# Performance work log

Hardware: AMD Instinct MI355X
Metric: run time of the kernel (lower is better)

## Reference

```python
import jax, jax.numpy as jnp
import numpy as np

V_IPC, N_ROLES, D = 50000, 16, 256
B, L = 2048, 64
F_BIB, H1, H2, D_OUT = 512, 1024, 1024, 512
N_EXP, N_CLS = 8, 10
LN_EPS = 1e-5


def setup_inputs() -> dict:
    key = jax.random.key(0)
    ks = jax.random.split(key, 24)
    s = 0.05
    ipc_emb = jax.random.normal(ks[0], (V_IPC, D), jnp.float32) * s
    ipc_emb = ipc_emb.at[0].set(0.0)  # padding_idx=0
    role_emb = jax.random.normal(ks[1], (N_ROLES, D), jnp.float32) * s
    role_emb = role_emb.at[0].set(0.0)
    inp = {
        "ipc_indices": jax.random.randint(ks[2], (B, L), 0, V_IPC),
        "role_indices": jax.random.randint(ks[3], (B, L), 0, N_ROLES),
        "bibliometric_features": jax.random.normal(ks[4], (B, F_BIB), jnp.float32),
        "ipc_padding_mask": jax.random.randint(ks[5], (B, L), 0, 2).astype(jnp.int32),
        "top_k": 2,
        "ipc_emb": ipc_emb,
        "role_emb": role_emb,
        "Wq": jax.random.normal(ks[6], (D, D), jnp.float32) * s,
        "bq": jnp.zeros((D,), jnp.float32),
        "Wk": jax.random.normal(ks[7], (D, D), jnp.float32) * s,
        "bk": jnp.zeros((D,), jnp.float32),
        "Wv": jax.random.normal(ks[8], (D, D), jnp.float32) * s,
        "bv": jnp.zeros((D,), jnp.float32),
        "global_context": jax.random.normal(ks[9], (D,), jnp.float32) * s,
        "ln_g": jnp.ones((D,), jnp.float32),
        "ln_b": jnp.zeros((D,), jnp.float32),
        "gate_W": jax.random.normal(ks[10], (D, N_EXP), jnp.float32) * s,
        "gate_b": jnp.zeros((N_EXP,), jnp.float32),
        "expert_biases": jnp.zeros((N_EXP,), jnp.float32),
        "W1": jax.random.normal(ks[11], (N_EXP, F_BIB, H1), jnp.float32) * s,
        "b1": jnp.zeros((N_EXP, H1), jnp.float32),
        "W2": jax.random.normal(ks[12], (N_EXP, H1, H2), jnp.float32) * s,
        "b2": jnp.zeros((N_EXP, H2), jnp.float32),
        "W3": jax.random.normal(ks[13], (N_EXP, H2, D_OUT), jnp.float32) * s,
        "b3": jnp.zeros((N_EXP, D_OUT), jnp.float32),
        "head_W": jax.random.normal(ks[14], (D_OUT, N_CLS), jnp.float32) * s,
        "head_b": jnp.zeros((N_CLS,), jnp.float32),
    }
    return inp


def reference(ipc_indices, role_indices, bibliometric_features, ipc_padding_mask, top_k,
              ipc_emb, role_emb, Wq, bq, Wk, bk, Wv, bv, global_context, ln_g, ln_b,
              gate_W, gate_b, expert_biases, W1, b1, W2, b2, W3, b3, head_W, head_b):
    # embeddings + role combine  -> [B, L, D]
    x = ipc_emb[ipc_indices] + role_emb[role_indices]
    # attention pooling with a global learned query (same query for every batch row)
    keys = x @ Wk + bk                                  # [B, L, D]
    values = x @ Wv + bv                                # [B, L, D]
    q = global_context @ Wq + bq                        # [D]
    scores = jnp.einsum('d,bld->bl', q, keys)           # [B, L]
    scores = jnp.where(ipc_padding_mask == 0, -1e9, scores)
    attn = jax.nn.softmax(scores, axis=-1)              # [B, L]
    pooled = jnp.einsum('bl,bld->bd', attn, values)     # [B, D]
    mu = pooled.mean(-1, keepdims=True)
    var = ((pooled - mu) ** 2).mean(-1, keepdims=True)
    router_in = (pooled - mu) / jnp.sqrt(var + LN_EPS) * ln_g + ln_b
    # router: select with biased scores, gate with unbiased scores
    affinity = router_in @ gate_W + gate_b              # [B, E]
    sel_scores = affinity + expert_biases
    _, idx = jax.lax.top_k(sel_scores, top_k)           # [B, K]
    gw = jax.nn.softmax(jnp.take_along_axis(affinity, idx, axis=-1), axis=-1)  # [B, K]
    # dense all-expert MLP (reference form of masked per-expert loop)
    h = jax.nn.relu(jnp.einsum('bi,eih->ebh', bibliometric_features, W1) + b1[:, None, :])
    h = jax.nn.relu(jnp.einsum('ebh,ehj->ebj', h, W2) + b2[:, None, :])
    eo = jnp.einsum('ebj,ejo->ebo', h, W3) + b3[:, None, :]  # [E, B, O]
    # gather each token's top-k expert outputs and combine
    bidx = jnp.arange(idx.shape[0])[:, None]            # [B, 1]
    sel_out = eo[idx, bidx]                             # [B, K, O]
    moe_out = jnp.einsum('bk,bko->bo', gw, sel_out)     # [B, O]
    logits = moe_out @ head_W + head_b                  # [B, n_classes]
    return logits, idx
```

## Files before the change

kernel.cpp:

```cpp
#include <hip/hip_runtime.h>
#include <hip/hip_bf16.h>
#include <math.h>


#define LN_EPS 1e-5f

typedef __bf16 bf16_t;
typedef __bf16 bf16x8 __attribute__((ext_vector_type(8)));
typedef float f32x4 __attribute__((ext_vector_type(4)));

__global__ __launch_bounds__(256)
void prep_kq(const float* __restrict__ Wq, const float* __restrict__ bq,
             const float* __restrict__ Wk, const float* __restrict__ bk,
             const float* __restrict__ gc, float* __restrict__ kq_out) {
  __shared__ float q[256];
  __shared__ float red[4];
  const int t = threadIdx.x, bi = blockIdx.x;
  float s = bq[t];
  for (int d = 0; d < 256; d++) s += gc[d] * Wq[d * 256 + t];
  q[t] = s;
  __syncthreads();
  const int rl = t >> 5, sl = t & 31;
  const int r = bi * 8 + rl;
  float p = 0.f;
#pragma unroll
  for (int i = 0; i < 8; i++) { const int d = sl + 32 * i; p += Wk[r * 256 + d] * q[d]; }
#pragma unroll
  for (int o = 16; o > 0; o >>= 1) p += __shfl_down(p, o, 32);
  if (sl == 0) kq_out[r] = p;
  if (bi == 0) {
    float z = q[t] * bk[t];
    const int lane = t & 63, wave = t >> 6;
#pragma unroll
    for (int o = 32; o > 0; o >>= 1) z += __shfl_down(z, o);
    if (lane == 0) red[wave] = z;
    __syncthreads();
    if (t == 0) kq_out[256] = red[0] + red[1] + red[2] + red[3];
  }
}

__global__ __launch_bounds__(256)
void transpose_ft(const float* __restrict__ W1, const float* __restrict__ W2,
                  const float* __restrict__ W3, bf16_t* __restrict__ B1,
                  bf16_t* __restrict__ B2, bf16_t* __restrict__ B3) {
  __shared__ float tile[64][65];
  const int z = blockIdx.z;
  const float* W; bf16_t* Bft; int K, N, e;
  if (z < 8)       { W = W1; Bft = B1; K = 512;  N = 1024; e = z; }
  else if (z < 16) { W = W2; Bft = B2; K = 1024; N = 1024; e = z - 8; }
  else             { W = W3; Bft = B3; K = 1024; N = 512;  e = z - 16; }
  const int n0 = blockIdx.x * 64, k0 = blockIdx.y * 64;
  if (n0 >= N || k0 >= K) return;
  const float* Wp = W + (size_t)e * K * N;
  bf16_t* Bp = Bft + (size_t)e * N * K;
  const int tq = threadIdx.x & 15, th = threadIdx.x >> 4;
#pragma unroll
  for (int i = 0; i < 4; i++) {
    const int row = th + 16 * i;
    *(float4*)&tile[row][tq * 4] = *(const float4*)(Wp + (size_t)(k0 + row) * N + n0 + tq * 4);
  }
  __syncthreads();
  const int lane = threadIdx.x & 63, sub = threadIdx.x >> 6;
  const int nk = K >> 5;
#pragma unroll
  for (int it = 0; it < 2; it++) {
    const int fid = sub + it * 4;
    const int ntl = fid & 3, ktl = fid >> 2;
    const int n_l = ntl * 16 + (lane & 15);
    const int k_l = ktl * 32 + (lane >> 4) * 8;
    bf16x8 o;
#pragma unroll
    for (int j = 0; j < 8; j++) o[j] = (bf16_t)tile[k_l + j][n_l];
    const size_t idx = ((((size_t)(n0 >> 4) + ntl) * nk + (k0 >> 5) + ktl) * 64 + lane) * 8;
    *(bf16x8*)(Bp + idx) = o;
  }
}

__global__ __launch_bounds__(256)
void score_tab_kernel(const float* __restrict__ ipc_emb,
                      const float* __restrict__ role_emb,
                      const float* __restrict__ kq_qbk, float* __restrict__ tab) {
  const int wave = threadIdx.x >> 6, lane = threadIdx.x & 63;
  const float4 kq = *(const float4*)(kq_qbk + lane * 4);
  const int base = (blockIdx.x * 4 + wave) * 32;
  for (int i = 0; i < 32; i++) {
    const int r = base + i;
    if (r >= 50016) return;
    const float* src = (r < 50000) ? (ipc_emb + (size_t)r * 256)
                                   : (role_emb + (size_t)(r - 50000) * 256);
    const float4 v = *(const float4*)(src + lane * 4);
    float p = v.x * kq.x + v.y * kq.y + v.z * kq.z + v.w * kq.w;
#pragma unroll
    for (int o = 32; o > 0; o >>= 1) p += __shfl_down(p, o);
    if (lane == 0) tab[r] = (r < 50000) ? p : (p + kq_qbk[256]);
  }
}

__global__ __launch_bounds__(256)
void xbar_kernel(const int* __restrict__ ipc_idx, const int* __restrict__ role_idx,
                 const int* __restrict__ maskp,
                 const float* __restrict__ ipc_emb, const float* __restrict__ role_emb,
                 const float* __restrict__ tab, float* __restrict__ xbar_g) {
  const int b = blockIdx.x;
  __shared__ float attn_s[64];
  __shared__ __align__(16) float part[4][256];
  const int t = threadIdx.x, wave = t >> 6, lane = t & 63;
  const int d0 = lane * 4;
  if (wave == 0) {
    const int ii = ipc_idx[b * 64 + lane], ri = role_idx[b * 64 + lane];
    float s = tab[ii] + tab[50000 + ri];
    s = (maskp[b * 64 + lane] == 0) ? -1e9f : s;
    float m = s;
#pragma unroll
    for (int o = 32; o > 0; o >>= 1) m = fmaxf(m, __shfl_xor(m, o));
    const float ev = expf(s - m);
    float sum = ev;
#pragma unroll
    for (int o = 32; o > 0; o >>= 1) sum += __shfl_xor(sum, o);
    attn_s[lane] = ev / sum;
  }
  __syncthreads();
  float p0 = 0.f, p1 = 0.f, p2 = 0.f, p3 = 0.f;
  for (int l = wave; l < 64; l += 4) {
    const float a = attn_s[l];
    const int ii = ipc_idx[b * 64 + l], ri = role_idx[b * 64 + l];
    const float4 xe = *(const float4*)(ipc_emb + (size_t)ii * 256 + d0);
    const float4 re = *(const float4*)(role_emb + (size_t)ri * 256 + d0);
    p0 += a * (xe.x + re.x); p1 += a * (xe.y + re.y);
    p2 += a * (xe.z + re.z); p3 += a * (xe.w + re.w);
  }
  *(float4*)&part[wave][d0] = make_float4(p0, p1, p2, p3);
  __syncthreads();
  xbar_g[(size_t)b * 256 + t] = part[0][t] + part[1][t] + part[2][t] + part[3][t];
}

__global__ __launch_bounds__(256)
void pool_kernel(const float* __restrict__ xbar_g, const float* __restrict__ Wv,
                 const float* __restrict__ bvec,
                 const float* __restrict__ ln_g, const float* __restrict__ ln_b,
                 const float* __restrict__ gate_W, const float* __restrict__ gate_b,
                 const float* __restrict__ expert_biases,
                 float* __restrict__ out_idx_f, int* __restrict__ ws_idx,
                 float* __restrict__ ws_gw) {
  const int rb = blockIdx.x * 8;
  __shared__ __align__(16) float xs[8][256];
  __shared__ __align__(16) float ps[8][260];
  const int t = threadIdx.x, wave = t >> 6, lane = t & 63;
  for (int i = t; i < 512; i += 256)
    ((float4*)xs)[i] = ((const float4*)(xbar_g + (size_t)rb * 256))[i];
  __syncthreads();
  const float* x0 = xs[wave * 2];
  const float* x1 = xs[wave * 2 + 1];
  f32x4 acc0 = {0.f, 0.f, 0.f, 0.f}, acc1 = {0.f, 0.f, 0.f, 0.f};
  for (int d = 0; d < 256; d += 4) {
    const float4 xa = *(const float4*)(x0 + d);
    const float4 xb = *(const float4*)(x1 + d);
#pragma unroll
    for (int j = 0; j < 4; j++) {
      const float4 wv = *(const float4*)(Wv + (size_t)(d + j) * 256 + lane * 4);
      const float aj = (&xa.x)[j], bj = (&xb.x)[j];
      acc0.x += aj * wv.x; acc0.y += aj * wv.y; acc0.z += aj * wv.z; acc0.w += aj * wv.w;
      acc1.x += bj * wv.x; acc1.y += bj * wv.y; acc1.z += bj * wv.z; acc1.w += bj * wv.w;
    }
  }
  const float4 bvv = *(const float4*)(bvec + lane * 4);
  acc0.x += bvv.x; acc0.y += bvv.y; acc0.z += bvv.z; acc0.w += bvv.w;
  acc1.x += bvv.x; acc1.y += bvv.y; acc1.z += bvv.z; acc1.w += bvv.w;
  *(f32x4*)&ps[wave * 2][lane * 4] = acc0;
  *(f32x4*)&ps[wave * 2 + 1][lane * 4] = acc1;
  __syncthreads();
  const float4 lg = *(const float4*)(ln_g + lane * 4);
  const float4 lb = *(const float4*)(ln_b + lane * 4);
#pragma unroll
  for (int rr = 0; rr < 2; rr++) {
    const int r = wave * 2 + rr;
    const float4 v = *(const float4*)&ps[r][lane * 4];
    float s1 = v.x + v.y + v.z + v.w;
#pragma unroll
    for (int o = 32; o > 0; o >>= 1) s1 += __shfl_xor(s1, o);
    const float mu = s1 * (1.f / 256.f);
    const float4 df = make_float4(v.x - mu, v.y - mu, v.z - mu, v.w - mu);
    float s2 = df.x * df.x + df.y * df.y + df.z * df.z + df.w * df.w;
#pragma unroll
    for (int o = 32; o > 0; o >>= 1) s2 += __shfl_xor(s2, o);
    const float inv = 1.f / sqrtf(s2 * (1.f / 256.f) + LN_EPS);
    f32x4 rv;
    rv[0] = df.x * inv * lg.x + lb.x; rv[1] = df.y * inv * lg.y + lb.y;
    rv[2] = df.z * inv * lg.z + lb.z; rv[3] = df.w * inv * lg.w + lb.w;
    f32x4 pa = {0.f, 0.f, 0.f, 0.f}, pb = {0.f, 0.f, 0.f, 0.f};
#pragma unroll
    for (int k = 0; k < 4; k++) {
      const int d = lane * 4 + k;
      const f32x4 g0 = *(const f32x4*)(gate_W + d * 8);
      const f32x4 g1 = *(const f32x4*)(gate_W + d * 8 + 4);
      pa += rv[k] * g0;
      pb += rv[k] * g1;
    }
#pragma unroll
    for (int o = 32; o > 0; o >>= 1) {
      pa[0] += __shfl_down(pa[0], o); pa[1] += __shfl_down(pa[1], o);
      pa[2] += __shfl_down(pa[2], o); pa[3] += __shfl_down(pa[3], o);
      pb[0] += __shfl_down(pb[0], o); pb[1] += __shfl_down(pb[1], o);
      pb[2] += __shfl_down(pb[2], o); pb[3] += __shfl_down(pb[3], o);
    }
    if (lane == 0) {
      float aff[8];
#pragma unroll
      for (int j = 0; j < 4; j++) { aff[j] = pa[j] + gate_b[j]; aff[4 + j] = pb[j] + gate_b[4 + j]; }
      float b0 = -1e30f; int i0 = 0;
#pragma unroll
      for (int j = 0; j < 8; j++) {
        const float s = aff[j] + expert_biases[j];
        if (s > b0) { b0 = s; i0 = j; }
      }
      float b1v = -1e30f; int i1 = 0;
#pragma unroll
      for (int j = 0; j < 8; j++) {
        const float s = aff[j] + expert_biases[j];
        if (j != i0 && s > b1v) { b1v = s; i1 = j; }
      }
      const float a0 = aff[i0], a1 = aff[i1];
      const float m = fmaxf(a0, a1);
      const float e0 = expf(a0 - m), e1 = expf(a1 - m);
      const float invs = 1.f / (e0 + e1);
      const int bg = rb + r;
      ws_idx[bg * 2] = i0; ws_idx[bg * 2 + 1] = i1;
      ws_gw[bg * 2] = e0 * invs; ws_gw[bg * 2 + 1] = e1 * invs;
      out_idx_f[bg * 2] = (float)i0; out_idx_f[bg * 2 + 1] = (float)i1;
    }
  }
}

__global__ __launch_bounds__(256)
void pack_kernel(const int* __restrict__ ws_idx, int* __restrict__ list_token,
                 int* __restrict__ a_of, int* __restrict__ offsets_g) {
  __shared__ int cnt[8]; __shared__ int off[9]; __shared__ int fill[8];
  const int t = threadIdx.x;
  if (t < 8) cnt[t] = 0;
  __syncthreads();
  for (int a = t; a < 4096; a += 256) atomicAdd(&cnt[ws_idx[a]], 1);
  __syncthreads();
  if (t == 0) {
    off[0] = 0;
    for (int e = 0; e < 8; e++) off[e + 1] = off[e] + ((cnt[e] + 63) & ~63);
  }
  __syncthreads();
  if (t < 8) fill[t] = off[t];
  if (t < 9) offsets_g[t] = off[t];
  for (int a = t; a < 4608; a += 256) list_token[a] = 0;
  __syncthreads();
  for (int a = t; a < 4096; a += 256) {
    const int e = ws_idx[a];
    const int pos = atomicAdd(&fill[e], 1);
    list_token[pos] = a >> 1;
    a_of[a] = pos;
  }
}

__global__ __launch_bounds__(64)
void gather_bib(const float* __restrict__ bib, const int* __restrict__ list_token,
                bf16_t* __restrict__ Xc) {
  const int a = blockIdx.x;
  const int tok = list_token[a];
  const int t = threadIdx.x;
  const float4 v1 = *(const float4*)(bib + (size_t)tok * 512 + t * 8);
  const float4 v2 = *(const float4*)(bib + (size_t)tok * 512 + t * 8 + 4);
  bf16x8 o;
  o[0] = (bf16_t)v1.x; o[1] = (bf16_t)v1.y; o[2] = (bf16_t)v1.z; o[3] = (bf16_t)v1.w;
  o[4] = (bf16_t)v2.x; o[5] = (bf16_t)v2.y; o[6] = (bf16_t)v2.z; o[7] = (bf16_t)v2.w;
  *(bf16x8*)(Xc + (size_t)a * 512 + t * 8) = o;
}

template <int K, int NT, bool RELU, typename OUT_T>
__global__ __launch_bounds__(256)
void expert_gemm_ft(const bf16_t* __restrict__ A, const bf16_t* __restrict__ Bft,
                    const float* __restrict__ bias, OUT_T* __restrict__ C,
                    const int* __restrict__ offsets) {
  constexpr int nk = K / 32;
  const int e = blockIdx.z;
  const int seg_hi = offsets[e + 1];
  const int blk_row = offsets[e] + blockIdx.y * 128;
  if (blk_row >= seg_hi) return;
  const int wave = threadIdx.x >> 6, lane = threadIdx.x & 63;
  const int row0 = blk_row + wave * 32;
  if (row0 >= seg_hi) return;
  const int n0 = blockIdx.x * 64;
  const bf16_t* Ap = A + (size_t)(row0 + (lane & 15)) * K + ((lane >> 4) * 8);
  const bf16_t* Bp = Bft + (size_t)e * NT * K + ((size_t)(n0 >> 4) * nk * 512 + lane * 8);
  f32x4 acc[2][4];
#pragma unroll
  for (int i = 0; i < 2; i++)
#pragma unroll
    for (int j = 0; j < 4; j++) acc[i][j] = (f32x4){0.f, 0.f, 0.f, 0.f};
  bf16x8 aX[2][2], bX[2][4];
#pragma unroll
  for (int mi = 0; mi < 2; mi++) aX[0][mi] = *(const bf16x8*)(Ap + mi * 16 * K);
#pragma unroll
  for (int ni = 0; ni < 4; ni++) bX[0][ni] = *(const bf16x8*)(Bp + (size_t)ni * nk * 512);
#pragma unroll
  for (int kt = 0; kt < nk; kt++) {
    const int cur = kt & 1, nxt = cur ^ 1;
    if (kt + 1 < nk) {
#pragma unroll
      for (int mi = 0; mi < 2; mi++)
        aX[nxt][mi] = *(const bf16x8*)(Ap + mi * 16 * K + (kt + 1) * 32);
#pragma unroll
      for (int ni = 0; ni < 4; ni++)
        bX[nxt][ni] = *(const bf16x8*)(Bp + ((size_t)ni * nk + kt + 1) * 512);
    }
#pragma unroll
    for (int mi = 0; mi < 2; mi++)
#pragma unroll
      for (int ni = 0; ni < 4; ni++)
        acc[mi][ni] = __builtin_amdgcn_mfma_f32_16x16x32_bf16(aX[cur][mi], bX[cur][ni], acc[mi][ni], 0, 0, 0);
  }
  const int fr = lane & 15, q = lane >> 4;
#pragma unroll
  for (int ni = 0; ni < 4; ni++) {
    const int col = n0 + ni * 16 + fr;
    const float bv = bias[e * NT + col];
#pragma unroll
    for (int mi = 0; mi < 2; mi++) {
#pragma unroll
      for (int r = 0; r < 4; r++) {
        const int row = row0 + mi * 16 + q * 4 + r;
        float v = acc[mi][ni][r] + bv;
        if (RELU) v = fmaxf(v, 0.f);
        C[(size_t)row * NT + col] = (OUT_T)v;
      }
    }
  }
}

__global__ __launch_bounds__(256)
void head_kernel(const float* __restrict__ O, const int* __restrict__ a_of,
                 const float* __restrict__ ws_gw, const float* __restrict__ head_W,
                 const float* __restrict__ head_b, float* __restrict__ out) {
  const int b = blockIdx.x, t = threadIdx.x;
  __shared__ float m[512];
  const int a0 = a_of[b * 2], a1 = a_of[b * 2 + 1];
  const float g0 = ws_gw[b * 2], g1 = ws_gw[b * 2 + 1];
  for (int d = t; d < 512; d += 256)
    m[d] = g0 * O[(size_t)a0 * 512 + d] + g1 * O[(size_t)a1 * 512 + d];
  __syncthreads();
  if (t < 160) {
    const int c = t >> 4, ch = t & 15;
    float p = 0.f;
#pragma unroll
    for (int i = 0; i < 32; i++) {
      const int d = i * 16 + ch;
      p += m[d] * head_W[d * 10 + c];
    }
#pragma unroll
    for (int o = 8; o > 0; o >>= 1) p += __shfl_down(p, o, 16);
    if (ch == 0) out[b * 10 + c] = p + head_b[c];
  }
}

extern "C" void kernel_launch(void* const* d_in, const int* in_sizes, int n_in,
                              void* d_out, int out_size, void* d_ws, size_t ws_size,
                              hipStream_t stream) {
  const int* ipc_idx = (const int*)d_in[0];
  const int* role_idx = (const int*)d_in[1];
  const float* bib = (const float*)d_in[2];
  const int* maskp = (const int*)d_in[3];
  const float* ipc_emb = (const float*)d_in[5];
  const float* role_emb = (const float*)d_in[6];
  const float* Wq = (const float*)d_in[7];
  const float* bq = (const float*)d_in[8];
  const float* Wk = (const float*)d_in[9];
  const float* bk = (const float*)d_in[10];
  const float* Wv = (const float*)d_in[11];
  const float* bv = (const float*)d_in[12];
  const float* gc = (const float*)d_in[13];
  const float* ln_g = (const float*)d_in[14];
  const float* ln_b = (const float*)d_in[15];
  const float* gate_W = (const float*)d_in[16];
  const float* gate_b = (const float*)d_in[17];
  const float* exp_b = (const float*)d_in[18];
  const float* W1 = (const float*)d_in[19];
  const float* b1 = (const float*)d_in[20];
  const float* W2 = (const float*)d_in[21];
  const float* b2 = (const float*)d_in[22];
  const float* W3 = (const float*)d_in[23];
  const float* b3 = (const float*)d_in[24];
  const float* head_W = (const float*)d_in[25];
  const float* head_b = (const float*)d_in[26];

  char* ws = (char*)d_ws;
  size_t off = 0;
  auto alloc = [&](size_t bytes) -> char* {
    char* p = ws + off;
    off += (bytes + 255) & ~(size_t)255;
    return p;
  };
  float* kq_qbk = (float*)alloc(257 * 4);
  float* tab = (float*)alloc(50016 * 4);
  float* xbar_g = (float*)alloc((size_t)2048 * 256 * 4);
  int* ws_idx = (int*)alloc(4096 * 4);
  float* ws_gw = (float*)alloc(4096 * 4);
  int* list_tok = (int*)alloc(4608 * 4);
  int* a_of = (int*)alloc(4096 * 4);
  int* offs = (int*)alloc(9 * 4);
  bf16_t* W1t = (bf16_t*)alloc((size_t)8 * 1024 * 512 * 2);
  bf16_t* W2t = (bf16_t*)alloc((size_t)8 * 1024 * 1024 * 2);
  bf16_t* W3t = (bf16_t*)alloc((size_t)8 * 512 * 1024 * 2);
  bf16_t* Xc = (bf16_t*)alloc((size_t)4608 * 512 * 2);
  bf16_t* H1c = (bf16_t*)alloc((size_t)4608 * 1024 * 2);
  bf16_t* H2c = (bf16_t*)alloc((size_t)4608 * 1024 * 2);
  float* Oc = (float*)alloc((size_t)4608 * 512 * 4);
  (void)in_sizes; (void)n_in; (void)out_size; (void)ws_size;

  float* out_logits = (float*)d_out;
  float* out_idx = (float*)d_out + 20480;

  prep_kq<<<32, 256, 0, stream>>>(Wq, bq, Wk, bk, gc, kq_qbk);
  transpose_ft<<<dim3(16, 16, 24), 256, 0, stream>>>(W1, W2, W3, W1t, W2t, W3t);
  score_tab_kernel<<<391, 256, 0, stream>>>(ipc_emb, role_emb, kq_qbk, tab);
  xbar_kernel<<<2048, 256, 0, stream>>>(ipc_idx, role_idx, maskp, ipc_emb, role_emb,
                                        tab, xbar_g);
  pool_kernel<<<256, 256, 0, stream>>>(xbar_g, Wv, bv, ln_g, ln_b, gate_W, gate_b,
                                       exp_b, out_idx, ws_idx, ws_gw);
  pack_kernel<<<1, 256, 0, stream>>>(ws_idx, list_tok, a_of, offs);
  gather_bib<<<4608, 64, 0, stream>>>(bib, list_tok, Xc);
  expert_gemm_ft<512, 1024, true, bf16_t><<<dim3(16, 36, 8), 256, 0, stream>>>(Xc, W1t, b1, H1c, offs);
  expert_gemm_ft<1024, 1024, true, bf16_t><<<dim3(16, 36, 8), 256, 0, stream>>>(H1c, W2t, b2, H2c, offs);
  expert_gemm_ft<1024, 512, false, float><<<dim3(8, 36, 8), 256, 0, stream>>>(H2c, W3t, b3, Oc, offs);
  head_kernel<<<2048, 256, 0, stream>>>(Oc, a_of, ws_gw, head_W, head_b, out_logits);
}
```

Baseline: 384.4 us.

## Fuse bib gather into first expert GEMM, merge prep into transpose, skip masked rows

Removes the gather_bib kernel and its bf16 staging buffer: the first expert GEMM now reads fp32 bibliometric rows through the token list and converts them to bf16 in registers before the MFMA. The prep_kq work is folded into the transpose launch as an extra z-slice, saving one launch. In the xbar kernel, rows with zero attention weight skip their embedding loads. In exchange, the first GEMM reads twice as many bytes per A element from scattered rows, and each N-tile block reloads the same fp32 rows.

```diff
diff --git a/kernel.cpp b/kernel.cpp
--- a/kernel.cpp
+++ b/kernel.cpp
@@ -9,42 +9,54 @@
 typedef __bf16 bf16x8 __attribute__((ext_vector_type(8)));
 typedef float f32x4 __attribute__((ext_vector_type(4)));
 
-__global__ __launch_bounds__(256)
-void prep_kq(const float* __restrict__ Wq, const float* __restrict__ bq,
-             const float* __restrict__ Wk, const float* __restrict__ bk,
-             const float* __restrict__ gc, float* __restrict__ kq_out) {
-  __shared__ float q[256];
-  __shared__ float red[4];
-  const int t = threadIdx.x, bi = blockIdx.x;
-  float s = bq[t];
-  for (int d = 0; d < 256; d++) s += gc[d] * Wq[d * 256 + t];
-  q[t] = s;
-  __syncthreads();
-  const int rl = t >> 5, sl = t & 31;
-  const int r = bi * 8 + rl;
-  float p = 0.f;
-#pragma unroll
-  for (int i = 0; i < 8; i++) { const int d = sl + 32 * i; p += Wk[r * 256 + d] * q[d]; }
-#pragma unroll
-  for (int o = 16; o > 0; o >>= 1) p += __shfl_down(p, o, 32);
-  if (sl == 0) kq_out[r] = p;
-  if (bi == 0) {
-    float z = q[t] * bk[t];
-    const int lane = t & 63, wave = t >> 6;
-#pragma unroll
-    for (int o = 32; o > 0; o >>= 1) z += __shfl_down(z, o);
-    if (lane == 0) red[wave] = z;
-    __syncthreads();
-    if (t == 0) kq_out[256] = red[0] + red[1] + red[2] + red[3];
-  }
-}
-
-__global__ __launch_bounds__(256)
-void transpose_ft(const float* __restrict__ W1, const float* __restrict__ W2,
-                  const float* __restrict__ W3, bf16_t* __restrict__ B1,
-                  bf16_t* __restrict__ B2, bf16_t* __restrict__ B3) {
+struct f4x2 { float4 a, b; };
+__device__ __forceinline__ f4x2 ldA8(const float* p) {
+  f4x2 v; v.a = *(const float4*)p; v.b = *(const float4*)(p + 4); return v;
+}
+__device__ __forceinline__ bf16x8 cvt8(const f4x2& v) {
+  bf16x8 o;
+  o[0] = (bf16_t)v.a.x; o[1] = (bf16_t)v.a.y; o[2] = (bf16_t)v.a.z; o[3] = (bf16_t)v.a.w;
+  o[4] = (bf16_t)v.b.x; o[5] = (bf16_t)v.b.y; o[6] = (bf16_t)v.b.z; o[7] = (bf16_t)v.b.w;
+  return o;
+}
+
+__global__ __launch_bounds__(256)
+void transpose_prep(const float* __restrict__ W1, const float* __restrict__ W2,
+                    const float* __restrict__ W3, bf16_t* __restrict__ B1,
+                    bf16_t* __restrict__ B2, bf16_t* __restrict__ B3,
+                    const float* __restrict__ Wq, const float* __restrict__ bq,
+                    const float* __restrict__ Wk, const float* __restrict__ bk,
+                    const float* __restrict__ gc, float* __restrict__ kq_out) {
   __shared__ float tile[64][65];
   const int z = blockIdx.z;
+  if (z == 24) {
+    if (blockIdx.y >= 2) return;
+    float* q = &tile[0][0];
+    float* red = &tile[0][0] + 256;
+    const int t = threadIdx.x, bi = blockIdx.y * 16 + blockIdx.x;
+    float s = bq[t];
+    for (int d = 0; d < 256; d++) s += gc[d] * Wq[d * 256 + t];
+    q[t] = s;
+    __syncthreads();
+    const int rl = t >> 5, sl = t & 31;
+    const int r = bi * 8 + rl;
+    float p = 0.f;
+#pragma unroll
+    for (int i = 0; i < 8; i++) { const int d = sl + 32 * i; p += Wk[r * 256 + d] * q[d]; }
+#pragma unroll
+    for (int o = 16; o > 0; o >>= 1) p += __shfl_down(p, o, 32);
+    if (sl == 0) kq_out[r] = p;
+    if (bi == 0) {
+      float z2 = q[t] * bk[t];
+      const int lane = t & 63, wave = t >> 6;
+#pragma unroll
+      for (int o = 32; o > 0; o >>= 1) z2 += __shfl_down(z2, o);
+      if (lane == 0) red[wave] = z2;
+      __syncthreads();
+      if (t == 0) kq_out[256] = red[0] + red[1] + red[2] + red[3];
+    }
+    return;
+  }
   const float* W; bf16_t* Bft; int K, N, e;
   if (z < 8)       { W = W1; Bft = B1; K = 512;  N = 1024; e = z; }
   else if (z < 16) { W = W2; Bft = B2; K = 1024; N = 1024; e = z - 8; }
@@ -123,6 +135,7 @@
   float p0 = 0.f, p1 = 0.f, p2 = 0.f, p3 = 0.f;
   for (int l = wave; l < 64; l += 4) {
     const float a = attn_s[l];
+    if (a == 0.f) continue;
     const int ii = ipc_idx[b * 64 + l], ri = role_idx[b * 64 + l];
     const float4 xe = *(const float4*)(ipc_emb + (size_t)ii * 256 + d0);
     const float4 re = *(const float4*)(role_emb + (size_t)ri * 256 + d0);
@@ -257,18 +270,67 @@
   }
 }
 
-__global__ __launch_bounds__(64)
-void gather_bib(const float* __restrict__ bib, const int* __restrict__ list_token,
-                bf16_t* __restrict__ Xc) {
-  const int a = blockIdx.x;
-  const int tok = list_token[a];
-  const int t = threadIdx.x;
-  const float4 v1 = *(const float4*)(bib + (size_t)tok * 512 + t * 8);
-  const float4 v2 = *(const float4*)(bib + (size_t)tok * 512 + t * 8 + 4);
-  bf16x8 o;
-  o[0] = (bf16_t)v1.x; o[1] = (bf16_t)v1.y; o[2] = (bf16_t)v1.z; o[3] = (bf16_t)v1.w;
-  o[4] = (bf16_t)v2.x; o[5] = (bf16_t)v2.y; o[6] = (bf16_t)v2.z; o[7] = (bf16_t)v2.w;
-  *(bf16x8*)(Xc + (size_t)a * 512 + t * 8) = o;
+template <int NT, bool RELU>
+__global__ __launch_bounds__(256)
+void expert_gemm_g1(const float* __restrict__ bib, const int* __restrict__ list_token,
+                    const bf16_t* __restrict__ Bft, const float* __restrict__ bias,
+                    bf16_t* __restrict__ C, const int* __restrict__ offsets) {
+  constexpr int K = 512, nk = K / 32;
+  const int e = blockIdx.z;
+  const int seg_hi = offsets[e + 1];
+  const int blk_row = offsets[e] + blockIdx.y * 128;
+  if (blk_row >= seg_hi) return;
+  const int wave = threadIdx.x >> 6, lane = threadIdx.x & 63;
+  const int row0 = blk_row + wave * 32;
+  if (row0 >= seg_hi) return;
+  const int n0 = blockIdx.x * 64;
+  const int tok0 = list_token[row0 + (lane & 15)];
+  const int tok1 = list_token[row0 + 16 + (lane & 15)];
+  const float* Ap0 = bib + (size_t)tok0 * 512 + (lane >> 4) * 8;
+  const float* Ap1 = bib + (size_t)tok1 * 512 + (lane >> 4) * 8;
+  const bf16_t* Bp = Bft + (size_t)e * NT * K + ((size_t)(n0 >> 4) * nk * 512 + lane * 8);
+  f32x4 acc[2][4];
+#pragma unroll
+  for (int i = 0; i < 2; i++)
+#pragma unroll
+    for (int j = 0; j < 4; j++) acc[i][j] = (f32x4){0.f, 0.f, 0.f, 0.f};
+  f4x2 aS[2][2]; bf16x8 bX[2][4];
+  aS[0][0] = ldA8(Ap0); aS[0][1] = ldA8(Ap1);
+#pragma unroll
+  for (int ni = 0; ni < 4; ni++) bX[0][ni] = *(const bf16x8*)(Bp + (size_t)ni * nk * 512);
+#pragma unroll
+  for (int kt = 0; kt < nk; kt++) {
+    const int cur = kt & 1, nxt = cur ^ 1;
+    if (kt + 1 < nk) {
+      aS[nxt][0] = ldA8(Ap0 + (kt + 1) * 32);
+      aS[nxt][1] = ldA8(Ap1 + (kt + 1) * 32);
+#pragma unroll
+      for (int ni = 0; ni < 4; ni++)
+        bX[nxt][ni] = *(const bf16x8*)(Bp + ((size_t)ni * nk + kt + 1) * 512);
+    }
+    const bf16x8 a0 = cvt8(aS[cur][0]), a1 = cvt8(aS[cur][1]);
+#pragma unroll
+    for (int ni = 0; ni < 4; ni++) {
+      acc[0][ni] = __builtin_amdgcn_mfma_f32_16x16x32_bf16(a0, bX[cur][ni], acc[0][ni], 0, 0, 0);
+      acc[1][ni] = __builtin_amdgcn_mfma_f32_16x16x32_bf16(a1, bX[cur][ni], acc[1][ni], 0, 0, 0);
+    }
+  }
+  const int fr = lane & 15, q = lane >> 4;
+#pragma unroll
+  for (int ni = 0; ni < 4; ni++) {
+    const int col = n0 + ni * 16 + fr;
+    const float bv = bias[e * NT + col];
+#pragma unroll
+    for (int mi = 0; mi < 2; mi++) {
+#pragma unroll
+      for (int r = 0; r < 4; r++) {
+        const int row = row0 + mi * 16 + q * 4 + r;
+        float v = acc[mi][ni][r] + bv;
+        if (RELU) v = fmaxf(v, 0.f);
+        C[(size_t)row * NT + col] = (bf16_t)v;
+      }
+    }
+  }
 }
 
 template <int K, int NT, bool RELU, typename OUT_T>
@@ -405,7 +467,6 @@
   bf16_t* W1t = (bf16_t*)alloc((size_t)8 * 1024 * 512 * 2);
   bf16_t* W2t = (bf16_t*)alloc((size_t)8 * 1024 * 1024 * 2);
   bf16_t* W3t = (bf16_t*)alloc((size_t)8 * 512 * 1024 * 2);
-  bf16_t* Xc = (bf16_t*)alloc((size_t)4608 * 512 * 2);
   bf16_t* H1c = (bf16_t*)alloc((size_t)4608 * 1024 * 2);
   bf16_t* H2c = (bf16_t*)alloc((size_t)4608 * 1024 * 2);
   float* Oc = (float*)alloc((size_t)4608 * 512 * 4);
@@ -414,16 +475,15 @@
   float* out_logits = (float*)d_out;
   float* out_idx = (float*)d_out + 20480;
 
-  prep_kq<<<32, 256, 0, stream>>>(Wq, bq, Wk, bk, gc, kq_qbk);
-  transpose_ft<<<dim3(16, 16, 24), 256, 0, stream>>>(W1, W2, W3, W1t, W2t, W3t);
+  transpose_prep<<<dim3(16, 16, 25), 256, 0, stream>>>(W1, W2, W3, W1t, W2t, W3t,
+                                                       Wq, bq, Wk, bk, gc, kq_qbk);
   score_tab_kernel<<<391, 256, 0, stream>>>(ipc_emb, role_emb, kq_qbk, tab);
   xbar_kernel<<<2048, 256, 0, stream>>>(ipc_idx, role_idx, maskp, ipc_emb, role_emb,
                                         tab, xbar_g);
   pool_kernel<<<256, 256, 0, stream>>>(xbar_g, Wv, bv, ln_g, ln_b, gate_W, gate_b,
                                        exp_b, out_idx, ws_idx, ws_gw);
   pack_kernel<<<1, 256, 0, stream>>>(ws_idx, list_tok, a_of, offs);
-  gather_bib<<<4608, 64, 0, stream>>>(bib, list_tok, Xc);
-  expert_gemm_ft<512, 1024, true, bf16_t><<<dim3(16, 36, 8), 256, 0, stream>>>(Xc, W1t, b1, H1c, offs);
+  expert_gemm_g1<1024, true><<<dim3(16, 36, 8), 256, 0, stream>>>(bib, list_tok, W1t, b1, H1c, offs);
   expert_gemm_ft<1024, 1024, true, bf16_t><<<dim3(16, 36, 8), 256, 0, stream>>>(H1c, W2t, b2, H2c, offs);
   expert_gemm_ft<1024, 512, false, float><<<dim3(8, 36, 8), 256, 0, stream>>>(H2c, W3t, b3, Oc, offs);
   head_kernel<<<2048, 256, 0, stream>>>(Oc, a_of, ws_gw, head_W, head_b, out_logits);
```

Result: no change. 379.7 us (-1.2%).
